# Optimization experiments

Measured on AMD Instinct MI355X. Metric: run time of the kernel, lower is better.

Reference implementation:

```python
import jax, jax.numpy as jnp
import numpy as np

B, N, DIN, DOUT, DA = 8, 2048, 128, 128, 2
NEG_SLOPE = 0.2


def setup_inputs() -> dict:
    key = jax.random.key(0)
    k = jax.random.split(key, 7)
    x = jax.random.normal(k[0], (B, N, DIN), dtype=jnp.float32)
    mask = jax.random.randint(k[1], (B, N, N), 0, 2, dtype=jnp.int32)
    s = 1.0 / np.sqrt(DIN)
    Wr = jax.random.uniform(k[2], (DA, DIN), jnp.float32, -s, s)      # linear_row.weight
    Wc = jax.random.uniform(k[3], (DA, DIN), jnp.float32, -s, s)      # linear_col.weight
    sa = 1.0 / np.sqrt(2 * DA)
    Wcat = jax.random.uniform(k[4], (2 * DA,), jnp.float32, -sa, sa)  # linear_concat.weight [1, 2*DA] flattened
    Wx = jax.random.uniform(k[5], (DOUT, DIN), jnp.float32, -s, s)    # linear_x.weight
    bx = jax.random.uniform(k[6], (DOUT,), jnp.float32, -s, s)        # linear_x.bias
    return {"x": x, "mask": mask, "Wr": Wr, "Wc": Wc, "Wcat": Wcat, "Wx": Wx, "bx": bx}


def reference(x, mask, Wr, Wc, Wcat, Wx, bx):
    # Row/col projections to tiny attention dim: [B, N, DA]
    row = jnp.einsum('bnd,ad->bna', x, Wr)
    col = jnp.einsum('bnd,ad->bna', x, Wc)
    # Concat scoring: e_ij = linear_concat(LeakyReLU(cat(row_i, col_j)))
    # decomposes as a1 . LR(row_i) + a2 . LR(col_j) -- avoids materializing [B,N,N,2*DA]
    a1, a2 = Wcat[:DA], Wcat[DA:]
    lr_row = jax.nn.leaky_relu(row, NEG_SLOPE) @ a1   # [B, N]
    lr_col = jax.nn.leaky_relu(col, NEG_SLOPE) @ a2   # [B, N]
    e = lr_row[:, :, None] + lr_col[:, None, :]       # [B, N, N]
    # Masked softmax over columns j
    e = jnp.where(mask > 0, e, jnp.float32(-1e9))
    atten = jax.nn.softmax(e, axis=-1)                # [B, N, N]
    # Value projection + combine
    xv = jnp.einsum('bnd,od->bno', x, Wx) + bx        # [B, N, DOUT]
    out = jnp.einsum('bij,bjo->bio', atten, xv)       # [B, N, DOUT]
    return out
```

## Files before the change

### kernel.cpp

```cpp
#include <hip/hip_runtime.h>


typedef __bf16 bf16x8 __attribute__((ext_vector_type(8)));
typedef __bf16 bf16x4 __attribute__((ext_vector_type(4)));
typedef float  f32x4  __attribute__((ext_vector_type(4)));
typedef int    i32x4  __attribute__((ext_vector_type(4)));
typedef unsigned int u32;

#define MFMA_BF16(a, b, c) __builtin_amdgcn_mfma_f32_16x16x32_bf16((a), (b), (c), 0, 0, 0)

#define GLOAD_LDS16(gp, lp)                                                     \
  __builtin_amdgcn_global_load_lds(                                             \
      (const __attribute__((address_space(1))) void*)(gp),                      \
      (__attribute__((address_space(3))) void*)(lp), 16, 0, 0)

static __device__ __forceinline__ bf16x8 cvt8(f32x4 a, f32x4 b) {
  bf16x8 r;
  r[0] = (__bf16)a[0]; r[1] = (__bf16)a[1]; r[2] = (__bf16)a[2]; r[3] = (__bf16)a[3];
  r[4] = (__bf16)b[0]; r[5] = (__bf16)b[1]; r[6] = (__bf16)b[2]; r[7] = (__bf16)b[3];
  return r;
}

__global__ __launch_bounds__(256) void prep_kernel(
    const float* __restrict__ x, const float* __restrict__ Wc,
    const float* __restrict__ Wcat, const float* __restrict__ Wx,
    const float* __restrict__ bx, __bf16* __restrict__ u)
{
  __shared__ __bf16 lds[9216];
  const int blk = blockIdx.x;
  const int b = blk >> 5, mt = blk & 31;
  const int wv = threadIdx.x >> 6, lane = threadIdx.x & 63;
  const int np = lane & 15, G = lane >> 4;
  const int r0 = mt * 64 + wv * 16;

  const float* xp = x + ((size_t)(b * 2048 + r0 + np)) * 128 + G * 8;
  bf16x8 af[4];
#pragma unroll
  for (int kk = 0; kk < 4; ++kk) {
    f32x4 x0 = *(const f32x4*)(xp + kk * 32);
    f32x4 x1 = *(const f32x4*)(xp + kk * 32 + 4);
    af[kk] = cvt8(x0, x1);
  }

  f32x4 acc[8], accC;
#pragma unroll
  for (int n = 0; n < 8; ++n) { acc[n][0] = 0.f; acc[n][1] = 0.f; acc[n][2] = 0.f; acc[n][3] = 0.f; }
  accC[0] = accC[1] = accC[2] = accC[3] = 0.f;

#pragma unroll
  for (int n = 0; n < 8; ++n) {
    const float* wp = Wx + (n * 16 + np) * 128 + G * 8;
#pragma unroll
    for (int kk = 0; kk < 4; ++kk) {
      f32x4 w0 = *(const f32x4*)(wp + kk * 32);
      f32x4 w1 = *(const f32x4*)(wp + kk * 32 + 4);
      acc[n] = MFMA_BF16(af[kk], cvt8(w0, w1), acc[n]);
    }
  }
#pragma unroll
  for (int kk = 0; kk < 4; ++kk) {
    bf16x8 bf;
    if (np < 2) {
      const float* cp = Wc + np * 128 + kk * 32 + G * 8;
      f32x4 c0 = *(const f32x4*)cp;
      f32x4 c1 = *(const f32x4*)(cp + 4);
      bf = cvt8(c0, c1);
    } else {
#pragma unroll
      for (int j = 0; j < 8; ++j) bf[j] = (__bf16)0.0f;
    }
    accC = MFMA_BF16(af[kk], bf, accC);
  }

  const float a20 = Wcat[2], a21 = Wcat[3];
  float wexp[4];
#pragma unroll
  for (int r = 0; r < 4; ++r) {
    float c0 = __shfl(accC[r], lane & 48);
    float c1 = __shfl(accC[r], (lane & 48) | 1);
    c0 = c0 > 0.f ? c0 : 0.2f * c0;
    c1 = c1 > 0.f ? c1 : 0.2f * c1;
    wexp[r] = __expf(c0 * a20 + c1 * a21);
  }

  const int t_rel = wv >> 1;
  const int g_store = (wv & 1) * 2 + (G >> 1);
  const int j0 = (G & 1) * 4;
#pragma unroll
  for (int n = 0; n < 8; ++n) {
    float bxv = bx[n * 16 + np];
    bf16x4 v;
#pragma unroll
    for (int r = 0; r < 4; ++r) v[r] = (__bf16)(wexp[r] * (acc[n][r] + bxv));
    *(bf16x4*)(&lds[(t_rel * 9 + n) * 512 + g_store * 128 + np * 8 + j0]) = v;
  }
  {
    bf16x4 v8;
#pragma unroll
    for (int r = 0; r < 4; ++r) v8[r] = (np == 0) ? (__bf16)wexp[r] : (__bf16)0.0f;
    *(bf16x4*)(&lds[(t_rel * 9 + 8) * 512 + g_store * 128 + np * 8 + j0]) = v8;
  }
  __syncthreads();
  __bf16* dst = u + ((size_t)(b * 64 + mt * 2)) * 9 * 512;
  for (int s = threadIdx.x; s < 1152; s += 256)
    ((i32x4*)dst)[s] = ((const i32x4*)lds)[s];
}

__global__ __launch_bounds__(256) void attn_kernel(
    const int* __restrict__ mask, const __bf16* __restrict__ u,
    float* __restrict__ out)
{
  __shared__ int smask[2 * 4096];
  const int b = blockIdx.x & 7, rt = blockIdx.x >> 3;
  const int wv = threadIdx.x >> 6, lane = threadIdx.x & 63;
  const int np = lane & 15, G = lane >> 4;
  const int row0 = rt * 32;
  const int n0 = wv * 2, n1 = n0 + 1;
  const int swz = (np & 7) << 2;
  const int hl = lane >> 5, cb = (lane & 31) * 16;

  const char* gbase = (const char*)(mask + ((size_t)b * 2048 + row0) * 2048);
  const __bf16* up = u + (size_t)b * 64 * 9 * 512 + lane * 8;

  f32x4 acc[2][3];
#pragma unroll
  for (int mi = 0; mi < 2; ++mi)
#pragma unroll
    for (int n = 0; n < 3; ++n) { acc[mi][n][0] = 0.f; acc[mi][n][1] = 0.f; acc[mi][n][2] = 0.f; acc[mi][n][3] = 0.f; }

#define STAGE(it, nb)                                                          \
  do {                                                                         \
    char* lbase = (char*)smask + (nb) * 16384 + wv * 4096;                     \
    _Pragma("unroll")                                                          \
    for (int i = 0; i < 4; ++i) {                                              \
      int lr = wv * 8 + i * 2 + hl;                                            \
      const char* gp = gbase + (size_t)lr * 8192 + (it) * 512 +                \
                       (cb ^ (((i * 2 + hl) & 7) << 4));                       \
      GLOAD_LDS16(gp, lbase + i * 1024);                                       \
    }                                                                          \
  } while (0)

  STAGE(0, 0);
  __syncthreads();

  for (int it = 0; it < 16; ++it) {
    if (it < 15) STAGE(it + 1, (it + 1) & 1);
    const u32* cur = (const u32*)smask + (it & 1) * 4096;
#pragma unroll
    for (int tk = 0; tk < 4; ++tk) {
      const int t = it * 4 + tk;
      const __bf16* ut = up + (size_t)(t * 9) * 512;
      bf16x8 U0 = *(const bf16x8*)(ut + n0 * 512);
      bf16x8 U1 = *(const bf16x8*)(ut + n1 * 512);
      bf16x8 UD = *(const bf16x8*)(ut + 8 * 512);
      const int X = tk * 32 + G * 8;
#pragma unroll
      for (int mi = 0; mi < 2; ++mi) {
        const u32* rp = cur + (mi * 16 + np) * 128;
        i32x4 ma = *(const i32x4*)(rp + (X ^ swz));
        i32x4 mb = *(const i32x4*)(rp + ((X + 4) ^ swz));
        union { u32 w[4]; bf16x8 v; } A;
        A.w[0] = (ma[0] ? 0x3F80u : 0u) | (ma[1] ? 0x3F800000u : 0u);
        A.w[1] = (ma[2] ? 0x3F80u : 0u) | (ma[3] ? 0x3F800000u : 0u);
        A.w[2] = (mb[0] ? 0x3F80u : 0u) | (mb[1] ? 0x3F800000u : 0u);
        A.w[3] = (mb[2] ? 0x3F80u : 0u) | (mb[3] ? 0x3F800000u : 0u);
        acc[mi][0] = MFMA_BF16(A.v, U0, acc[mi][0]);
        acc[mi][1] = MFMA_BF16(A.v, U1, acc[mi][1]);
        acc[mi][2] = MFMA_BF16(A.v, UD, acc[mi][2]);
      }
    }
    __syncthreads();
  }
#undef STAGE

#pragma unroll
  for (int mi = 0; mi < 2; ++mi) {
#pragma unroll
    for (int r = 0; r < 4; ++r) {
      float den = __shfl(acc[mi][2][r], lane & 48);
      float inv = 1.0f / den;
      float* op = out + ((size_t)b * 2048 + row0 + mi * 16 + 4 * G + r) * 128 + np;
      op[n0 * 16] = acc[mi][0][r] * inv;
      op[n1 * 16] = acc[mi][1][r] * inv;
    }
  }
}

extern "C" void kernel_launch(void* const* d_in, const int* in_sizes, int n_in,
                              void* d_out, int out_size, void* d_ws, size_t ws_size,
                              hipStream_t stream) {
  const float* x    = (const float*)d_in[0];
  const int*   mask = (const int*)d_in[1];
  const float* Wc   = (const float*)d_in[3];
  const float* Wcat = (const float*)d_in[4];
  const float* Wx   = (const float*)d_in[5];
  const float* bx   = (const float*)d_in[6];
  float* out = (float*)d_out;

  const size_t U_BYTES = (size_t)8 * 64 * 9 * 512 * 2;
  if (ws_size < U_BYTES) return;
  __bf16* u = (__bf16*)d_ws;

  prep_kernel<<<256, 256, 0, stream>>>(x, Wc, Wcat, Wx, bx, u);
  attn_kernel<<<512, 256, 0, stream>>>(mask, u, out);
}
```

Before: 227.5 us.

## Stage value tiles through LDS alongside mask with smaller pipeline steps

The attention kernel now loads the bf16 value/denominator tiles into LDS with async global-to-LDS copies in the same double-buffered stage as the mask, instead of reading them straight from global memory in the inner loop. The stage size is halved to 64 columns (32 iterations instead of 16), and the mask swizzle is recomputed for the narrower rows. The aim is to hide the value-load latency behind the pipeline. In exchange, LDS use rises to about 52 KB per block, which may lower occupancy, and the loop now needs twice as many barriers.

```diff
diff --git a/kernel.cpp b/kernel.cpp
--- a/kernel.cpp
+++ b/kernel.cpp
@@ -110,17 +110,19 @@
     const int* __restrict__ mask, const __bf16* __restrict__ u,
     float* __restrict__ out)
 {
-  __shared__ int smask[2 * 4096];
+  __shared__ char smem[2 * 26624];
   const int b = blockIdx.x & 7, rt = blockIdx.x >> 3;
   const int wv = threadIdx.x >> 6, lane = threadIdx.x & 63;
   const int np = lane & 15, G = lane >> 4;
   const int row0 = rt * 32;
   const int n0 = wv * 2, n1 = n0 + 1;
-  const int swz = (np & 7) << 2;
-  const int hl = lane >> 5, cb = (lane & 31) * 16;
-
-  const char* gbase = (const char*)(mask + ((size_t)b * 2048 + row0) * 2048);
-  const __bf16* up = u + (size_t)b * 64 * 9 * 512 + lane * 8;
+  const int swzB = (np & 7) << 4;
+
+  const char* gmask = (const char*)(mask + ((size_t)b * 2048 + row0) * 2048);
+  const char* gu = (const char*)(u + (size_t)b * 64 * 9 * 512);
+
+  const int mrow_g = G;
+  const int mbyte = np * 16;
 
   f32x4 acc[2][3];
 #pragma unroll
@@ -130,40 +132,45 @@
 
 #define STAGE(it, nb)                                                          \
   do {                                                                         \
-    char* lbase = (char*)smask + (nb) * 16384 + wv * 4096;                     \
+    char* mb_ = smem + (nb) * 26624;                                           \
+    char* ub_ = mb_ + 8192;                                                    \
     _Pragma("unroll")                                                          \
-    for (int i = 0; i < 4; ++i) {                                              \
-      int lr = wv * 8 + i * 2 + hl;                                            \
-      const char* gp = gbase + (size_t)lr * 8192 + (it) * 512 +                \
-                       (cb ^ (((i * 2 + hl) & 7) << 4));                       \
-      GLOAD_LDS16(gp, lbase + i * 1024);                                       \
+    for (int q = 0; q < 2; ++q) {               \
+      int i_ = wv * 2 + q;                                                     \
+      int row_ = i_ * 4 + mrow_g;                                              \
+      const char* gp = gmask + (size_t)row_ * 8192 + (it) * 256 +              \
+                       (mbyte ^ ((row_ & 7) << 4));                            \
+      GLOAD_LDS16(gp, mb_ + i_ * 1024);                                        \
+    }                                                                          \
+    for (int q = wv; q < 18; q += 4) {   \
+      const char* gp = gu + (size_t)(it) * 18432 + q * 1024 + lane * 16;       \
+      GLOAD_LDS16(gp, ub_ + q * 1024);                                         \
     }                                                                          \
   } while (0)
 
   STAGE(0, 0);
   __syncthreads();
 
-  for (int it = 0; it < 16; ++it) {
-    if (it < 15) STAGE(it + 1, (it + 1) & 1);
-    const u32* cur = (const u32*)smask + (it & 1) * 4096;
-#pragma unroll
-    for (int tk = 0; tk < 4; ++tk) {
-      const int t = it * 4 + tk;
-      const __bf16* ut = up + (size_t)(t * 9) * 512;
-      bf16x8 U0 = *(const bf16x8*)(ut + n0 * 512);
-      bf16x8 U1 = *(const bf16x8*)(ut + n1 * 512);
-      bf16x8 UD = *(const bf16x8*)(ut + 8 * 512);
-      const int X = tk * 32 + G * 8;
+  for (int it = 0; it < 32; ++it) {
+    if (it < 31) STAGE(it + 1, (it + 1) & 1);
+    const char* mb = smem + (it & 1) * 26624;
+    const char* ub = mb + 8192;
+#pragma unroll
+    for (int tk = 0; tk < 2; ++tk) {
+      bf16x8 U0 = *(const bf16x8*)(ub + tk * 9216 + n0 * 1024 + lane * 16);
+      bf16x8 U1 = *(const bf16x8*)(ub + tk * 9216 + n1 * 1024 + lane * 16);
+      bf16x8 UD = *(const bf16x8*)(ub + tk * 9216 + 8 * 1024 + lane * 16);
+      const int Xb = (tk * 32 + G * 8) * 4;
 #pragma unroll
       for (int mi = 0; mi < 2; ++mi) {
-        const u32* rp = cur + (mi * 16 + np) * 128;
-        i32x4 ma = *(const i32x4*)(rp + (X ^ swz));
-        i32x4 mb = *(const i32x4*)(rp + ((X + 4) ^ swz));
+        const char* rp = mb + (mi * 16 + np) * 256;
+        i32x4 ma = *(const i32x4*)(rp + (Xb ^ swzB));
+        i32x4 mz = *(const i32x4*)(rp + ((Xb + 16) ^ swzB));
         union { u32 w[4]; bf16x8 v; } A;
         A.w[0] = (ma[0] ? 0x3F80u : 0u) | (ma[1] ? 0x3F800000u : 0u);
         A.w[1] = (ma[2] ? 0x3F80u : 0u) | (ma[3] ? 0x3F800000u : 0u);
-        A.w[2] = (mb[0] ? 0x3F80u : 0u) | (mb[1] ? 0x3F800000u : 0u);
-        A.w[3] = (mb[2] ? 0x3F80u : 0u) | (mb[3] ? 0x3F800000u : 0u);
+        A.w[2] = (mz[0] ? 0x3F80u : 0u) | (mz[1] ? 0x3F800000u : 0u);
+        A.w[3] = (mz[2] ? 0x3F80u : 0u) | (mz[3] ? 0x3F800000u : 0u);
         acc[mi][0] = MFMA_BF16(A.v, U0, acc[mi][0]);
         acc[mi][1] = MFMA_BF16(A.v, U1, acc[mi][1]);
         acc[mi][2] = MFMA_BF16(A.v, UD, acc[mi][2]);
```

Measured after the change: 226.4 us. No clear change (-0.5%).

## Pre-pack mask into bf16 MFMA fragments in a separate kernel, deepen attn pipeline

Applied to the files above, without the earlier changes.

Adds a packA kernel that reads the int32 mask and writes it as bf16 0/1 values already laid out in MFMA A-fragment order into workspace. The attention kernel then streams these packed fragments plus the u tiles through a 4-deep LDS ring using global_load_lds and explicit vmcnt waits, so the inner loop no longer converts the mask. The mask is still read in full once, and the packed copy adds an extra 64MB write and read pass. The prep kernel's vector LDS stores are also split into scalar stores.

```diff
diff --git a/kernel.cpp b/kernel.cpp
--- a/kernel.cpp
+++ b/kernel.cpp
@@ -2,7 +2,6 @@
 
 
 typedef __bf16 bf16x8 __attribute__((ext_vector_type(8)));
-typedef __bf16 bf16x4 __attribute__((ext_vector_type(4)));
 typedef float  f32x4  __attribute__((ext_vector_type(4)));
 typedef int    i32x4  __attribute__((ext_vector_type(4)));
 typedef unsigned int u32;
@@ -89,16 +88,19 @@
 #pragma unroll
   for (int n = 0; n < 8; ++n) {
     float bxv = bx[n * 16 + np];
-    bf16x4 v;
+    __bf16 v[4];
 #pragma unroll
     for (int r = 0; r < 4; ++r) v[r] = (__bf16)(wexp[r] * (acc[n][r] + bxv));
-    *(bf16x4*)(&lds[(t_rel * 9 + n) * 512 + g_store * 128 + np * 8 + j0]) = v;
+    *(__bf16*)&lds[(t_rel * 9 + n) * 512 + g_store * 128 + np * 8 + j0 + 0] = v[0];
+    lds[(t_rel * 9 + n) * 512 + g_store * 128 + np * 8 + j0 + 1] = v[1];
+    lds[(t_rel * 9 + n) * 512 + g_store * 128 + np * 8 + j0 + 2] = v[2];
+    lds[(t_rel * 9 + n) * 512 + g_store * 128 + np * 8 + j0 + 3] = v[3];
   }
   {
-    bf16x4 v8;
-#pragma unroll
-    for (int r = 0; r < 4; ++r) v8[r] = (np == 0) ? (__bf16)wexp[r] : (__bf16)0.0f;
-    *(bf16x4*)(&lds[(t_rel * 9 + 8) * 512 + g_store * 128 + np * 8 + j0]) = v8;
+#pragma unroll
+    for (int r = 0; r < 4; ++r)
+      lds[(t_rel * 9 + 8) * 512 + g_store * 128 + np * 8 + j0 + r] =
+          (np == 0) ? (__bf16)wexp[r] : (__bf16)0.0f;
   }
   __syncthreads();
   __bf16* dst = u + ((size_t)(b * 64 + mt * 2)) * 9 * 512;
@@ -106,21 +108,63 @@
     ((i32x4*)dst)[s] = ((const i32x4*)lds)[s];
 }
 
+__global__ __launch_bounds__(256) void packA_kernel(
+    const int* __restrict__ mask, __bf16* __restrict__ Abuf)
+{
+  __shared__ int sm[32 * 129];
+  const int b = blockIdx.x & 7, rt = blockIdx.x >> 3;
+  const int tid = threadIdx.x;
+  const int* mbase = mask + ((size_t)b * 2048 + rt * 32) * 2048;
+  __bf16* obase = Abuf + (size_t)(b * 64 + rt) * 64 * 1024;
+
+  const int row_r = tid >> 3;
+  const int cb8 = (tid & 7) * 16;
+  const int f = tid >> 5;
+  const int tk = f >> 1, mi = f & 1;
+
+  for (int ch = 0; ch < 16; ++ch) {
+    const int* rp = mbase + (size_t)row_r * 2048 + ch * 128 + cb8;
+    i32x4 v0 = *(const i32x4*)rp;
+    i32x4 v1 = *(const i32x4*)(rp + 4);
+    i32x4 v2 = *(const i32x4*)(rp + 8);
+    i32x4 v3 = *(const i32x4*)(rp + 12);
+    __syncthreads();
+    *(i32x4*)&sm[row_r * 129 + cb8 + 0]  = v0;
+    *(i32x4*)&sm[row_r * 129 + cb8 + 4]  = v1;
+    *(i32x4*)&sm[row_r * 129 + cb8 + 8]  = v2;
+    *(i32x4*)&sm[row_r * 129 + cb8 + 12] = v3;
+    __syncthreads();
+#pragma unroll
+    for (int h = 0; h < 2; ++h) {
+      const int l = (tid & 31) + h * 32;
+      const int row = mi * 16 + (l & 15);
+      const int col = tk * 32 + (l >> 4) * 8;
+      u32 P[4];
+#pragma unroll
+      for (int q = 0; q < 4; ++q) {
+        u32 lo = sm[row * 129 + col + 2 * q]     ? 0x3F80u : 0u;
+        u32 hi = sm[row * 129 + col + 2 * q + 1] ? 0x3F800000u : 0u;
+        P[q] = lo | hi;
+      }
+      __bf16* op = obase + ((size_t)(ch * 4 + tk) * 2 + mi) * 512 + l * 8;
+      *(i32x4*)op = *(const i32x4*)P;
+    }
+  }
+}
+
 __global__ __launch_bounds__(256) void attn_kernel(
-    const int* __restrict__ mask, const __bf16* __restrict__ u,
+    const __bf16* __restrict__ Abuf, const __bf16* __restrict__ u,
     float* __restrict__ out)
 {
-  __shared__ int smask[2 * 4096];
+  __shared__ char smem[4 * 11264];
   const int b = blockIdx.x & 7, rt = blockIdx.x >> 3;
   const int wv = threadIdx.x >> 6, lane = threadIdx.x & 63;
   const int np = lane & 15, G = lane >> 4;
   const int row0 = rt * 32;
   const int n0 = wv * 2, n1 = n0 + 1;
-  const int swz = (np & 7) << 2;
-  const int hl = lane >> 5, cb = (lane & 31) * 16;
-
-  const char* gbase = (const char*)(mask + ((size_t)b * 2048 + row0) * 2048);
-  const __bf16* up = u + (size_t)b * 64 * 9 * 512 + lane * 8;
+
+  const char* gA = (const char*)Abuf + (size_t)(b * 64 + rt) * 64 * 2048;
+  const char* gu = (const char*)u + (size_t)b * 64 * 9216;
 
   f32x4 acc[2][3];
 #pragma unroll
@@ -130,48 +174,60 @@
 
 #define STAGE(it, nb)                                                          \
   do {                                                                         \
-    char* lbase = (char*)smask + (nb) * 16384 + wv * 4096;                     \
-    _Pragma("unroll")                                                          \
-    for (int i = 0; i < 4; ++i) {                                              \
-      int lr = wv * 8 + i * 2 + hl;                                            \
-      const char* gp = gbase + (size_t)lr * 8192 + (it) * 512 +                \
-                       (cb ^ (((i * 2 + hl) & 7) << 4));                       \
-      GLOAD_LDS16(gp, lbase + i * 1024);                                       \
+    char* dst = smem + (nb) * 11264;                                           \
+    if (wv == 0) {                                                             \
+      const char* ga = gA + (size_t)(it) * 2048 + lane * 16;                   \
+      GLOAD_LDS16(ga, dst);                                                    \
+      GLOAD_LDS16(ga + 1024, dst + 1024);                                      \
+      GLOAD_LDS16(gu + (size_t)(it) * 9216 + lane * 16, dst + 2048);           \
+    } else if (wv == 3) {                                                      \
+      const char* gp = gu + (size_t)(it) * 9216 + 7 * 1024 + lane * 16;        \
+      GLOAD_LDS16(gp, dst + 2048 + 7 * 1024);                                  \
+      GLOAD_LDS16(gp + 1024, dst + 2048 + 8 * 1024);                           \
+    } else {                                                                   \
+      const char* gp = gu + (size_t)(it) * 9216 + (wv * 3 - 2) * 1024 + lane * 16; \
+      GLOAD_LDS16(gp, dst + 2048 + (wv * 3 - 2) * 1024);                       \
+      GLOAD_LDS16(gp + 1024, dst + 2048 + (wv * 3 - 1) * 1024);                \
+      GLOAD_LDS16(gp + 2048, dst + 2048 + (wv * 3) * 1024);                    \
     }                                                                          \
   } while (0)
 
-  STAGE(0, 0);
-  __syncthreads();
-
-  for (int it = 0; it < 16; ++it) {
-    if (it < 15) STAGE(it + 1, (it + 1) & 1);
-    const u32* cur = (const u32*)smask + (it & 1) * 4096;
-#pragma unroll
-    for (int tk = 0; tk < 4; ++tk) {
-      const int t = it * 4 + tk;
-      const __bf16* ut = up + (size_t)(t * 9) * 512;
-      bf16x8 U0 = *(const bf16x8*)(ut + n0 * 512);
-      bf16x8 U1 = *(const bf16x8*)(ut + n1 * 512);
-      bf16x8 UD = *(const bf16x8*)(ut + 8 * 512);
-      const int X = tk * 32 + G * 8;
-#pragma unroll
-      for (int mi = 0; mi < 2; ++mi) {
-        const u32* rp = cur + (mi * 16 + np) * 128;
-        i32x4 ma = *(const i32x4*)(rp + (X ^ swz));
-        i32x4 mb = *(const i32x4*)(rp + ((X + 4) ^ swz));
-        union { u32 w[4]; bf16x8 v; } A;
-        A.w[0] = (ma[0] ? 0x3F80u : 0u) | (ma[1] ? 0x3F800000u : 0u);
-        A.w[1] = (ma[2] ? 0x3F80u : 0u) | (ma[3] ? 0x3F800000u : 0u);
-        A.w[2] = (mb[0] ? 0x3F80u : 0u) | (mb[1] ? 0x3F800000u : 0u);
-        A.w[3] = (mb[2] ? 0x3F80u : 0u) | (mb[3] ? 0x3F800000u : 0u);
-        acc[mi][0] = MFMA_BF16(A.v, U0, acc[mi][0]);
-        acc[mi][1] = MFMA_BF16(A.v, U1, acc[mi][1]);
-        acc[mi][2] = MFMA_BF16(A.v, UD, acc[mi][2]);
-      }
-    }
-    __syncthreads();
-  }
+#define CONSUME(nb)                                                            \
+  do {                                                                         \
+    const char* buf = smem + (nb) * 11264;                                     \
+    bf16x8 A0 = *(const bf16x8*)(buf + lane * 16);                             \
+    bf16x8 A1 = *(const bf16x8*)(buf + 1024 + lane * 16);                      \
+    const char* ub = buf + 2048;                                               \
+    bf16x8 U0 = *(const bf16x8*)(ub + n0 * 1024 + lane * 16);                  \
+    bf16x8 U1 = *(const bf16x8*)(ub + n1 * 1024 + lane * 16);                  \
+    bf16x8 UD = *(const bf16x8*)(ub + 8 * 1024 + lane * 16);                   \
+    acc[0][0] = MFMA_BF16(A0, U0, acc[0][0]);                                  \
+    acc[0][1] = MFMA_BF16(A0, U1, acc[0][1]);                                  \
+    acc[0][2] = MFMA_BF16(A0, UD, acc[0][2]);                                  \
+    acc[1][0] = MFMA_BF16(A1, U0, acc[1][0]);                                  \
+    acc[1][1] = MFMA_BF16(A1, U1, acc[1][1]);                                  \
+    acc[1][2] = MFMA_BF16(A1, UD, acc[1][2]);                                  \
+  } while (0)
+
+  STAGE(0, 0); STAGE(1, 1); STAGE(2, 2);
+  const int wvu = __builtin_amdgcn_readfirstlane(wv);
+
+  for (int it = 0; it <= 61; ++it) {
+    if (wvu == 3) asm volatile("s_waitcnt vmcnt(4)" ::: "memory");
+    else          asm volatile("s_waitcnt vmcnt(6)" ::: "memory");
+    __builtin_amdgcn_s_barrier();
+    CONSUME(it & 3);
+    if (it <= 60) STAGE(it + 3, (it + 3) & 3);
+  }
+  if (wvu == 3) asm volatile("s_waitcnt vmcnt(2)" ::: "memory");
+  else          asm volatile("s_waitcnt vmcnt(3)" ::: "memory");
+  __builtin_amdgcn_s_barrier();
+  CONSUME(62 & 3);
+  asm volatile("s_waitcnt vmcnt(0)" ::: "memory");
+  __builtin_amdgcn_s_barrier();
+  CONSUME(63 & 3);
 #undef STAGE
+#undef CONSUME
 
 #pragma unroll
   for (int mi = 0; mi < 2; ++mi) {
@@ -198,9 +254,12 @@
   float* out = (float*)d_out;
 
   const size_t U_BYTES = (size_t)8 * 64 * 9 * 512 * 2;
-  if (ws_size < U_BYTES) return;
-  __bf16* u = (__bf16*)d_ws;
+  const size_t A_BYTES = (size_t)8 * 2048 * 2048 * 2;
+  if (ws_size < U_BYTES + A_BYTES) return;
+  __bf16* u    = (__bf16*)d_ws;
+  __bf16* Abuf = (__bf16*)((char*)d_ws + U_BYTES);
 
   prep_kernel<<<256, 256, 0, stream>>>(x, Wc, Wcat, Wx, bx, u);
-  attn_kernel<<<512, 256, 0, stream>>>(mask, u, out);
-}
+  packA_kernel<<<512, 256, 0, stream>>>(mask, Abuf);
+  attn_kernel<<<512, 256, 0, stream>>>(Abuf, u, out);
+}
```

Result: slower. 251.3 us (+10.5%).
